# Performance work log

Measured on AMD Instinct MI355X. Metric: run time of the kernel, lower is better.

The kernel has to match this reference:

```python
import math
import jax, jax.numpy as jnp
import numpy as np

WS = 4            # window size
LS = 2 * WS       # local context size
NH = 8            # num heads
DIM = 128
EPS = 1e-5


def setup_inputs() -> dict:
    key = jax.random.key(0)
    ks = jax.random.split(key, 8)
    B, C, H, W = 4, DIM, 48, 48
    features = jax.random.normal(ks[0], (B, C, H, W), dtype=jnp.float32)
    s = 0.02
    return {
        'features': features,
        'ln_w': jnp.ones((C,), jnp.float32),
        'ln_b': jnp.zeros((C,), jnp.float32),
        'q_w': jax.random.normal(ks[1], (C, C), jnp.float32) * s,
        'q_b': jnp.zeros((C,), jnp.float32),
        'kv_w': jax.random.normal(ks[2], (2 * C, C), jnp.float32) * s,
        'kv_b': jnp.zeros((2 * C,), jnp.float32),
        'out_w': jax.random.normal(ks[3], (C, C), jnp.float32) * s,
        'out_b': jnp.zeros((C,), jnp.float32),
    }


def _avgpool_tokens(x, k):
    # x: [B,C,H,W] -> [B, (H//k)*(W//k), C]
    B, C, H, W = x.shape
    t = x.reshape(B, C, H // k, k, W // k, k).mean(axis=(3, 5))
    return t.reshape(B, C, -1).transpose(0, 2, 1)


def reference(features, ln_w, ln_b, q_w, q_b, kv_w, kv_b, out_w, out_b):
    B, C, H, W = features.shape
    Hw, Ww = H // WS, W // WS
    nw = Hw * Ww
    hd = C // NH

    # ---- window partition: [B,C,H,W] -> [B*nw, WS*WS, C]
    qt = features.reshape(B, C, Hw, WS, Ww, WS).transpose(0, 2, 4, 3, 5, 1)
    qt = qt.reshape(B * nw, WS * WS, C)

    # ---- LayerNorm(dim)
    mu = qt.mean(-1, keepdims=True)
    var = qt.var(-1, keepdims=True)
    qt = (qt - mu) / jnp.sqrt(var + EPS) * ln_w + ln_b

    # ---- local context: pad to target, unfold kernel=LS stride=WS
    target = (int(math.sqrt(nw)) - 1) * WS + LS
    ph, pw = max(0, target - H), max(0, target - W)
    pad = ((0, 0), (0, 0), (ph // 2, ph - ph // 2), (pw // 2, pw - pw // 2))
    padded = jnp.pad(features, pad)
    # channel order of patches is (C, kh, kw), same as torch unfold
    patches = jax.lax.conv_general_dilated_patches(
        padded, filter_shape=(LS, LS), window_strides=(WS, WS), padding='VALID')
    local = patches.reshape(B, C, LS * LS, nw).transpose(0, 3, 2, 1)
    local = local.reshape(B * nw, LS * LS, C)

    # ---- multi-scale pooled tokens, broadcast to each window
    mid = _avgpool_tokens(features, 2)      # [B, M, C]
    glo = _avgpool_tokens(features, 4)      # [B, G, C]
    mid = jnp.broadcast_to(mid[:, None], (B, nw) + mid.shape[1:]).reshape(B * nw, -1, C)
    glo = jnp.broadcast_to(glo[:, None], (B, nw) + glo.shape[1:]).reshape(B * nw, -1, C)

    kv_tokens = jnp.concatenate([local, mid, glo], axis=1)  # [B*nw, Nkv, C]

    # ---- projections (torch Linear: x @ W.T + b)
    queries = qt @ q_w.T + q_b
    kv = kv_tokens @ kv_w.T + kv_b
    keys, values = kv[..., :C], kv[..., C:]

    # ---- multi-head attention
    Nq, Nkv = queries.shape[1], keys.shape[1]
    q = queries.reshape(-1, Nq, NH, hd)
    k = keys.reshape(-1, Nkv, NH, hd)
    v = values.reshape(-1, Nkv, NH, hd)
    scores = jnp.einsum('bqhd,bkhd->bhqk', q, k) / math.sqrt(hd)
    weights = jax.nn.softmax(scores, axis=-1)
    attended = jnp.einsum('bhqk,bkhd->bqhd', weights, v).reshape(-1, Nq, C)

    out = attended @ out_w.T + out_b

    # ---- window reconstruction -> [B,C,H,W]
    out = out.reshape(B, Hw, Ww, WS, WS, C).transpose(0, 5, 1, 3, 2, 4)
    out = out.reshape(B, C, H, W)
    return out + features
```

## Files before the change

kernel.cpp:

```cpp
#include <hip/hip_runtime.h>


typedef unsigned short u16;
typedef short v8s __attribute__((ext_vector_type(8)));
typedef v8s __attribute__((may_alias)) v8s_am;
typedef short v4s __attribute__((ext_vector_type(4)));
typedef v4s __attribute__((may_alias)) v4s_am;
typedef float v4f __attribute__((ext_vector_type(4)));

#define MFMA_BF16(a, b, c) __builtin_amdgcn_mfma_f32_16x16x32_bf16(a, b, c, 0, 0, 0)

#if __has_builtin(__builtin_amdgcn_mfma_f32_16x16x16bf16_1k)
#define MFMA16(a, b, c) __builtin_amdgcn_mfma_f32_16x16x16bf16_1k(a, b, c, 0, 0, 0)
#else
static __device__ __forceinline__ v4f mfma16_fb(v4s a, v4s b, v4f c) {
    v8s a8 = {a[0], a[1], a[2], a[3], 0, 0, 0, 0};
    v8s b8 = {b[0], b[1], b[2], b[3], 0, 0, 0, 0};
    return MFMA_BF16(a8, b8, c);
}
#define MFMA16(a, b, c) mfma16_fb(a, b, c)
#endif

#if __has_builtin(__builtin_amdgcn_exp2f)
#define EXP2(x) __builtin_amdgcn_exp2f(x)
#else
#define EXP2(x) exp2f(x)
#endif

__device__ __forceinline__ float b2f(u16 u) {
    union { unsigned int i; float f; } x;
    x.i = ((unsigned int)u) << 16;
    return x.f;
}
__device__ __forceinline__ u16 f2b(float f) {
    union { float f; unsigned int i; } x;
    x.f = f;
    unsigned int u = x.i;
    return (u16)((u + 0x7fffu + ((u >> 16) & 1u)) >> 16);
}

__global__ __launch_bounds__(256) void k_prep(
    const float* __restrict__ F,
    const float* __restrict__ qw, const float* __restrict__ kvw,
    const float* __restrict__ ow,
    const float* __restrict__ lnw, const float* __restrict__ lnb,
    u16* __restrict__ Xt, u16* __restrict__ Wb, float* __restrict__ MuRs,
    u16* __restrict__ Pml)
{
    int blk = blockIdx.x;
    int t = threadIdx.x;
    if (blk >= 304) {
        int gid = (blk - 304) * 256 + t;
        int row = gid >> 4;
        int seg = gid & 15;
        v8s outv;
        if (row < 2304) {
            int b = row / 576, r = row % 576;
            int i = r / 24, j = r % 24;
#pragma unroll
            for (int jc = 0; jc < 8; ++jc) {
                int c = seg * 8 + jc;
                const float* src = F + ((size_t)(b * 128 + c)) * 2304 + (2 * i) * 48 + 2 * j;
                float2 a = *(const float2*)src;
                float2 d = *(const float2*)(src + 48);
                outv[jc] = (short)f2b((a.x + a.y + d.x + d.y) * 0.25f);
            }
        } else {
            int r2 = row - 2304;
            int b = r2 / 144, r = r2 % 144;
            int i = r / 12, j = r % 12;
#pragma unroll
            for (int jc = 0; jc < 8; ++jc) {
                int c = seg * 8 + jc;
                const float* src = F + ((size_t)(b * 128 + c)) * 2304 + (4 * i) * 48 + 4 * j;
                float s = 0.f;
#pragma unroll
                for (int di = 0; di < 4; ++di) {
                    float4 v = *(const float4*)(src + di * 48);
                    s += (v.x + v.y) + (v.z + v.w);
                }
                outv[jc] = (short)f2b(s * 0.0625f);
            }
        }
        *(v8s_am*)&Pml[((size_t)row) * 128 + seg * 8] = outv;
        return;
    }
    if (blk >= 288) {
        int base = (blk - 288) * 4096 + t * 16;
#pragma unroll
        for (int i = 0; i < 4; ++i) {
            int idx = base + i * 4;
            const float* src; int off;
            if (idx < 16384)      { src = qw;  off = idx; }
            else if (idx < 49152) { src = kvw; off = idx - 16384; }
            else                  { src = ow;  off = idx - 49152; }
            float4 v = *(const float4*)(src + off);
            unsigned long long packed =
                (unsigned long long)f2b(v.x) |
                ((unsigned long long)f2b(v.y) << 16) |
                ((unsigned long long)f2b(v.z) << 32) |
                ((unsigned long long)f2b(v.w) << 48);
            *(unsigned long long*)(Wb + idx) = packed;
        }
        if (blk == 288) {
            Wb[65536 + t] = f2b(t < 128 ? lnw[t] : lnb[t - 128]);
        }
        return;
    }
    __shared__ u16 X[128][34];
    int b = blk / 72;
    int p0 = (blk % 72) * 32;
#pragma unroll 4
    for (int i = 0; i < 16; ++i) {
        int c = i * 8 + (t >> 5);
        int pix = t & 31;
        X[c][pix] = f2b(F[((size_t)(b * 128 + c)) * 2304 + p0 + pix]);
    }
    __syncthreads();
    int pix = t >> 3;
    int c0 = (t & 7) * 16;
    size_t row = (size_t)(b * 2304 + p0 + pix) * 128;
    float s = 0.f, s2 = 0.f;
#pragma unroll
    for (int sg = 0; sg < 2; ++sg) {
        v8s raw;
#pragma unroll
        for (int j = 0; j < 8; ++j) {
            u16 u = X[c0 + sg * 8 + j][pix];
            raw[j] = (short)u;
            float v = b2f(u);
            s += v; s2 += v * v;
        }
        *(v8s_am*)&Xt[row + c0 + sg * 8] = raw;
    }
    s += __shfl_xor(s, 1);  s2 += __shfl_xor(s2, 1);
    s += __shfl_xor(s, 2);  s2 += __shfl_xor(s2, 2);
    s += __shfl_xor(s, 4);  s2 += __shfl_xor(s2, 4);
    if ((t & 7) == 0) {
        float mean = s * (1.f / 128.f);
        float var = s2 * (1.f / 128.f) - mean * mean;
        float rstd = rsqrtf(var + 1e-5f);
        MuRs[(b * 2304 + p0 + pix) * 2]     = mean;
        MuRs[(b * 2304 + p0 + pix) * 2 + 1] = rstd;
    }
}

__global__ __launch_bounds__(256) void k_gemm_kv(
    const u16* __restrict__ Pml,
    const u16* __restrict__ W,
    const float* __restrict__ bias,
    u16* __restrict__ KVh,
    u16* __restrict__ VTg)
{
    __shared__ u16 Al[64][136];
    __shared__ u16 Wl[64][136];
    int tm = blockIdx.x * 64, tn = blockIdx.y * 64;
    int t = threadIdx.x;
    {
        int seg = t & 15, r0 = t >> 4;
#pragma unroll
        for (int i = 0; i < 4; ++i) {
            int r = r0 + 16 * i;
            *(v8s_am*)&Al[r][seg * 8] = *(const v8s_am*)&Pml[((size_t)(tm + r)) * 128 + seg * 8];
            *(v8s_am*)&Wl[r][seg * 8] = *(const v8s_am*)&W[((size_t)(tn + r)) * 128 + seg * 8];
        }
    }
    __syncthreads();
    int lane = t & 63, wave = t >> 6;
    int n15 = lane & 15, quad = lane >> 4;
    int wm = (wave & 1) * 32, wn = (wave >> 1) * 32;
    v4f acc[2][2] = {};
#pragma unroll
    for (int kc = 0; kc < 4; ++kc) {
        v8s a[2], bb[2];
#pragma unroll
        for (int im = 0; im < 2; ++im)
            a[im] = *(const v8s_am*)&Al[wm + im * 16 + n15][kc * 32 + quad * 8];
#pragma unroll
        for (int in = 0; in < 2; ++in)
            bb[in] = *(const v8s_am*)&Wl[wn + in * 16 + n15][kc * 32 + quad * 8];
#pragma unroll
        for (int im = 0; im < 2; ++im)
#pragma unroll
            for (int in = 0; in < 2; ++in)
                acc[im][in] = MFMA_BF16(a[im], bb[in], acc[im][in]);
    }
#pragma unroll
    for (int in = 0; in < 2; ++in) {
        int n = tn + wn + in * 16 + n15;
        float bv = bias[n];
#pragma unroll
        for (int im = 0; im < 2; ++im) {
            int mbase = tm + wm + im * 16 + quad * 4;
#pragma unroll
            for (int r = 0; r < 4; ++r) {
                int m = mbase + r;
                u16 h = f2b(acc[im][in][r] + bv);
                if (n < 128) {
                    KVh[((size_t)(n >> 4) * 2880 + m) * 16 + (n & 15)] = h;
                } else {
                    int ch = n - 128, bb2, tok;
                    if (m < 2304) { bb2 = m / 576; tok = m % 576; }
                    else { int r2 = m - 2304; bb2 = r2 / 144; tok = 576 + r2 % 144; }
                    VTg[((size_t)(bb2 * 128 + ch)) * 720 + tok] = h;
                }
            }
        }
    }
}

__global__ __launch_bounds__(512, 2) void k_attn_fused(
    const float* __restrict__ F,
    const u16* __restrict__ Xt,
    const float* __restrict__ MuRs,
    const u16* __restrict__ KVh,
    const u16* __restrict__ VTg,
    const u16* __restrict__ Wb,
    const float* __restrict__ qb,
    const float* __restrict__ kvb,
    const float* __restrict__ ob,
    float* __restrict__ Out)
{
    __shared__ u16 KP[8][64][16];
    __shared__ u16 VtW[8][16][68];

    const u16* qwb  = Wb;
    const u16* kvwb = Wb + 16384;
    const u16* owb  = Wb + 49152;
    const u16* lnwb = Wb + 65536;
    const u16* lnbb = Wb + 65664;
    u16* Atp = &VtW[0][0][0];

    int blk = blockIdx.x;
    int xcd = blk & 7, jj = blk >> 3;
    int b = xcd >> 1;
    int wr = (xcd & 1) * 6 + jj / 12;
    int wc = jj % 12;

    int t = threadIdx.x;
    int lane = t & 63, wave = t >> 6, n15 = lane & 15, quad = lane >> 4;
    v8s zf8 = {};
    v4f zz4 = {0.f, 0.f, 0.f, 0.f};
    const float QSCALE = 0.25f * 1.44269504f;

    u16* KPw = &KP[wave][0][0];
    const u16* kwave = KVh + (size_t)wave * 46080;
    const u16* vrow0 = VTg + (size_t)b * 92160
                     + (size_t)(wave * 16 + n15) * 720 + quad * 4;

    v8s kN0, kN1;
    {
        const u16* s = kwave + (size_t)(b * 576 + lane) * 16;
        kN0 = *(const v8s_am*)s; kN1 = *(const v8s_am*)(s + 8);
    }

    int qh = wr * 4 + (n15 >> 2), qw_ = wc * 4 + (n15 & 3);
    int qpix = b * 2304 + qh * 48 + qw_;
    float mu = MuRs[qpix * 2], rstd = MuRs[qpix * 2 + 1];
    v8s xln[4];
#pragma unroll
    for (int kc = 0; kc < 4; ++kc) {
        v8s x  = *(const v8s_am*)&Xt[(size_t)qpix * 128 + kc * 32 + quad * 8];
        v8s lw = *(const v8s_am*)&lnwb[kc * 32 + quad * 8];
        v8s lb = *(const v8s_am*)&lnbb[kc * 32 + quad * 8];
        v8s y;
#pragma unroll
        for (int j = 0; j < 8; ++j)
            y[j] = (short)f2b((b2f((u16)x[j]) - mu) * rstd * b2f((u16)lw[j]) + b2f((u16)lb[j]));
        xln[kc] = y;
    }

    v4s qf;
    {
        int n0 = wave * 16;
        v4f qacc = zz4;
#pragma unroll
        for (int kc = 0; kc < 4; ++kc) {
            v8s aw = *(const v8s_am*)&qwb[((size_t)(n0 + n15)) * 128 + kc * 32 + quad * 8];
            qacc = MFMA_BF16(aw, xln[kc], qacc);
        }
#pragma unroll
        for (int r = 0; r < 4; ++r)
            qf[r] = (short)f2b((qacc[r] + qb[n0 + quad * 4 + r]) * QSCALE);
    }

    v4s kfloc[4];
#pragma unroll
    for (int g = 0; g < 4; ++g) {
        int tl = g * 16 + n15;
        int fh = tl >> 3, fw = tl & 7;
        int hh = wr * 4 - 2 + fh, ww = wc * 4 - 2 + fw;
        bool valid = (hh >= 0 && hh < 48 && ww >= 0 && ww < 48);
        size_t arow = (size_t)(b * 2304 + hh * 48 + ww) * 128;
        v8s xb[4];
#pragma unroll
        for (int kc = 0; kc < 4; ++kc) {
            v8s v = zf8;
            if (valid) v = *(const v8s_am*)&Xt[arow + kc * 32 + quad * 8];
            xb[kc] = v;
        }
#pragma unroll
        for (int s = 0; s < 2; ++s) {
            int sbase = s * 128 + wave * 16;
            v4f acc = zz4;
#pragma unroll
            for (int kc = 0; kc < 4; ++kc) {
                v8s aw = *(const v8s_am*)&kvwb[((size_t)(sbase + n15)) * 128 + kc * 32 + quad * 8];
                acc = MFMA_BF16(aw, xb[kc], acc);
            }
            if (s == 0) {
                v4s k4;
#pragma unroll
                for (int r = 0; r < 4; ++r)
                    k4[r] = (short)f2b(acc[r] + kvb[sbase + quad * 4 + r]);
                kfloc[g] = k4;
            } else {
#pragma unroll
                for (int r = 0; r < 4; ++r)
                    VtW[wave][quad * 4 + r][g * 16 + n15] =
                        f2b(acc[r] + kvb[sbase + quad * 4 + r]);
            }
        }
    }

    v4f oacc = zz4;
    float ls = 0.f;

    asm volatile("s_waitcnt lgkmcnt(0)" ::: "memory");
#pragma unroll
    for (int g = 0; g < 4; ++g) {
        v4f St = MFMA16(kfloc[g], qf, zz4);
        float p0 = EXP2(St[0]), p1 = EXP2(St[1]);
        float p2 = EXP2(St[2]), p3 = EXP2(St[3]);
        ls += (p0 + p1) + (p2 + p3);
        v4s pk = {(short)f2b(p0), (short)f2b(p1), (short)f2b(p2), (short)f2b(p3)};
        v4s vf = *(const v4s_am*)&VtW[wave][n15][g * 16 + quad * 4];
        oacc = MFMA16(vf, pk, oacc);
    }
    __syncthreads();

    *(v8s_am*)&KPw[lane * 16]     = kN0;
    *(v8s_am*)&KPw[lane * 16 + 8] = kN1;
    {
        const u16* s = kwave + (size_t)(b * 576 + 64 + lane) * 16;
        kN0 = *(const v8s_am*)s; kN1 = *(const v8s_am*)(s + 8);
    }

    for (int tb = 0; tb <= 10; ++tb) {
        v4s kf[4];
#pragma unroll
        for (int g = 0; g < 4; ++g)
            kf[g] = *(const v4s_am*)&KPw[(g * 16 + n15) * 16 + quad * 4];
        *(v8s_am*)&KPw[lane * 16]     = kN0;
        *(v8s_am*)&KPw[lane * 16 + 8] = kN1;
        if (tb < 10) {
            int t2 = tb + 2;
            int row = (t2 < 9) ? (b * 576 + t2 * 64 + lane)
                               : (2304 + b * 144 + (t2 - 9) * 64 + lane);
            if (t2 == 11) row = 2304 + b * 144 + 128 + n15;
            const u16* s = kwave + (size_t)row * 16;
            kN0 = *(const v8s_am*)s; kN1 = *(const v8s_am*)(s + 8);
        }
        v4s vp[4];
#pragma unroll
        for (int g = 0; g < 4; ++g)
            vp[g] = *(const v4s_am*)(vrow0 + tb * 64 + g * 16);
#pragma unroll
        for (int g = 0; g < 4; ++g) {
            v4f St = MFMA16(kf[g], qf, zz4);
            float p0 = EXP2(St[0]), p1 = EXP2(St[1]);
            float p2 = EXP2(St[2]), p3 = EXP2(St[3]);
            ls += (p0 + p1) + (p2 + p3);
            v4s pk = {(short)f2b(p0), (short)f2b(p1), (short)f2b(p2), (short)f2b(p3)};
            oacc = MFMA16(vp[g], pk, oacc);
        }
    }
    {
        v4s kf = *(const v4s_am*)&KPw[n15 * 16 + quad * 4];
        v4s vf = *(const v4s_am*)(vrow0 + 704);
        v4f St = MFMA16(kf, qf, zz4);
        float p0 = EXP2(St[0]), p1 = EXP2(St[1]);
        float p2 = EXP2(St[2]), p3 = EXP2(St[3]);
        ls += (p0 + p1) + (p2 + p3);
        v4s pk = {(short)f2b(p0), (short)f2b(p1), (short)f2b(p2), (short)f2b(p3)};
        oacc = MFMA16(vf, pk, oacc);
    }

    ls += __shfl_xor(ls, 16);
    ls += __shfl_xor(ls, 32);
    {
        float inv = 1.f / ls;
        v4s a4 = {(short)f2b(oacc[0] * inv), (short)f2b(oacc[1] * inv),
                  (short)f2b(oacc[2] * inv), (short)f2b(oacc[3] * inv)};
        *(v4s_am*)&Atp[n15 * 136 + wave * 16 + quad * 4] = a4;
    }
    __syncthreads();

    {
        int n0 = wave * 16;
        v4f oa = zz4;
#pragma unroll
        for (int kc = 0; kc < 4; ++kc) {
            v8s af = *(const v8s_am*)&Atp[n15 * 136 + kc * 32 + quad * 8];
            v8s bf = *(const v8s_am*)&owb[((size_t)(n0 + n15)) * 128 + kc * 32 + quad * 8];
            oa = MFMA_BF16(af, bf, oa);
        }
        int c = n0 + n15;
        float bv = ob[c];
#pragma unroll
        for (int r = 0; r < 4; ++r) {
            int pix = quad * 4 + r;
            int hh = wr * 4 + (pix >> 2), ww_ = wc * 4 + (pix & 3);
            size_t idx = ((size_t)(b * 128 + c)) * 2304 + hh * 48 + ww_;
            Out[idx] = oa[r] + bv + F[idx];
        }
    }
}

extern "C" void kernel_launch(void* const* d_in, const int* in_sizes, int n_in,
                              void* d_out, int out_size, void* d_ws, size_t ws_size,
                              hipStream_t stream)
{
    const float* F   = (const float*)d_in[0];
    const float* lnw = (const float*)d_in[1];
    const float* lnb = (const float*)d_in[2];
    const float* qw  = (const float*)d_in[3];
    const float* qb  = (const float*)d_in[4];
    const float* kvw = (const float*)d_in[5];
    const float* kvb = (const float*)d_in[6];
    const float* ow  = (const float*)d_in[7];
    const float* ob  = (const float*)d_in[8];
    float* Out = (float*)d_out;

    u16* ws    = (u16*)d_ws;
    u16* Xt    = ws;
    u16* Pml   = Xt + 9216 * 128;
    u16* KVh   = Pml + 2880 * 128;
    u16* VTg   = KVh + 8 * 2880 * 16;
    u16* Wb    = VTg + 4 * 128 * 720;
    float* MuRs = (float*)(Wb + 65792);
    u16* kvwb = Wb + 16384;

    k_prep<<<484, 256, 0, stream>>>(F, qw, kvw, ow, lnw, lnb, Xt, Wb, MuRs, Pml);
    k_gemm_kv<<<dim3(45, 4), 256, 0, stream>>>(Pml, kvwb, kvb, KVh, VTg);
    k_attn_fused<<<576, 512, 0, stream>>>(F, Xt, MuRs, KVh, VTg, Wb,
                                          qb, kvb, ob, Out);
}
```

Baseline: 129.1 us.

## Swizzle K LDS staging, prefetch V one tile ahead, raise occupancy bound

After: 131.7 us. 2.0% more time.

```diff
diff --git a/kernel.cpp b/kernel.cpp
--- a/kernel.cpp
+++ b/kernel.cpp
@@ -209,7 +209,7 @@
     }
 }
 
-__global__ __launch_bounds__(512, 2) void k_attn_fused(
+__global__ __launch_bounds__(512, 3) void k_attn_fused(
     const float* __restrict__ F,
     const u16* __restrict__ Xt,
     const float* __restrict__ MuRs,
@@ -243,7 +243,12 @@
     v4f zz4 = {0.f, 0.f, 0.f, 0.f};
     const float QSCALE = 0.25f * 1.44269504f;
 
-    u16* KPw = &KP[wave][0][0];
+    char* KPb = (char*)&KP[wave][0][0];
+    int swW = (lane & 7) << 4;
+    int wb0 = (lane * 32) ^ swW;
+    int wb1 = (lane * 32 + 16) ^ swW;
+    int rdb = (n15 * 32 + quad * 8) ^ ((n15 & 7) << 4);
+
     const u16* kwave = KVh + (size_t)wave * 46080;
     const u16* vrow0 = VTg + (size_t)b * 92160
                      + (size_t)(wave * 16 + n15) * 720 + quad * 4;
@@ -339,20 +344,23 @@
     }
     __syncthreads();
 
-    *(v8s_am*)&KPw[lane * 16]     = kN0;
-    *(v8s_am*)&KPw[lane * 16 + 8] = kN1;
+    *(v8s_am*)(KPb + wb0) = kN0;
+    *(v8s_am*)(KPb + wb1) = kN1;
     {
         const u16* s = kwave + (size_t)(b * 576 + 64 + lane) * 16;
         kN0 = *(const v8s_am*)s; kN1 = *(const v8s_am*)(s + 8);
     }
+    v4s vpC[4], vpN[4];
+#pragma unroll
+    for (int g = 0; g < 4; ++g) vpC[g] = *(const v4s_am*)(vrow0 + g * 16);
 
     for (int tb = 0; tb <= 10; ++tb) {
         v4s kf[4];
 #pragma unroll
         for (int g = 0; g < 4; ++g)
-            kf[g] = *(const v4s_am*)&KPw[(g * 16 + n15) * 16 + quad * 4];
-        *(v8s_am*)&KPw[lane * 16]     = kN0;
-        *(v8s_am*)&KPw[lane * 16 + 8] = kN1;
+            kf[g] = *(const v4s_am*)(KPb + rdb + g * 512);
+        *(v8s_am*)(KPb + wb0) = kN0;
+        *(v8s_am*)(KPb + wb1) = kN1;
         if (tb < 10) {
             int t2 = tb + 2;
             int row = (t2 < 9) ? (b * 576 + t2 * 64 + lane)
@@ -361,10 +369,14 @@
             const u16* s = kwave + (size_t)row * 16;
             kN0 = *(const v8s_am*)s; kN1 = *(const v8s_am*)(s + 8);
         }
-        v4s vp[4];
-#pragma unroll
-        for (int g = 0; g < 4; ++g)
-            vp[g] = *(const v4s_am*)(vrow0 + tb * 64 + g * 16);
+        {
+            int o1 = (tb == 10) ? 704 : (tb + 1) * 64;
+#pragma unroll
+            for (int g = 0; g < 4; ++g) {
+                int off = (tb == 10) ? 704 : (o1 + g * 16);
+                vpN[g] = *(const v4s_am*)(vrow0 + off);
+            }
+        }
 #pragma unroll
         for (int g = 0; g < 4; ++g) {
             v4f St = MFMA16(kf[g], qf, zz4);
@@ -372,18 +384,19 @@
             float p2 = EXP2(St[2]), p3 = EXP2(St[3]);
             ls += (p0 + p1) + (p2 + p3);
             v4s pk = {(short)f2b(p0), (short)f2b(p1), (short)f2b(p2), (short)f2b(p3)};
-            oacc = MFMA16(vp[g], pk, oacc);
-        }
-    }
-    {
-        v4s kf = *(const v4s_am*)&KPw[n15 * 16 + quad * 4];
-        v4s vf = *(const v4s_am*)(vrow0 + 704);
+            oacc = MFMA16(vpC[g], pk, oacc);
+        }
+#pragma unroll
+        for (int g = 0; g < 4; ++g) vpC[g] = vpN[g];
+    }
+    {
+        v4s kf = *(const v4s_am*)(KPb + rdb);
         v4f St = MFMA16(kf, qf, zz4);
         float p0 = EXP2(St[0]), p1 = EXP2(St[1]);
         float p2 = EXP2(St[2]), p3 = EXP2(St[3]);
         ls += (p0 + p1) + (p2 + p3);
         v4s pk = {(short)f2b(p0), (short)f2b(p1), (short)f2b(p2), (short)f2b(p3)};
-        oacc = MFMA16(vf, pk, oacc);
+        oacc = MFMA16(vpC[0], pk, oacc);
     }
 
     ls += __shfl_xor(ls, 16);
```

## Precompute local K/V projection per pixel once instead of per window

Applied to the files above, without the earlier changes.

New measurement: 121.6 us. 5.8% less time.

```diff
diff --git a/kernel.cpp b/kernel.cpp
--- a/kernel.cpp
+++ b/kernel.cpp
@@ -44,11 +44,25 @@
     const float* __restrict__ qw, const float* __restrict__ kvw,
     const float* __restrict__ ow,
     const float* __restrict__ lnw, const float* __restrict__ lnb,
+    const float* __restrict__ kvb,
     u16* __restrict__ Xt, u16* __restrict__ Wb, float* __restrict__ MuRs,
-    u16* __restrict__ Pml)
+    u16* __restrict__ Pml, u16* __restrict__ Vlh)
 {
     int blk = blockIdx.x;
     int t = threadIdx.x;
+    if (blk >= 484) {
+        int base = (blk - 484) * 8192 + t * 32;
+#pragma unroll
+        for (int k = 0; k < 4; ++k) {
+            int off = base + k * 8;
+            int ch = off / 10816;
+            u16 bv = f2b(kvb[128 + ch]);
+            v8s o = {(short)bv, (short)bv, (short)bv, (short)bv,
+                     (short)bv, (short)bv, (short)bv, (short)bv};
+            *(v8s_am*)&Vlh[off] = o;
+        }
+        return;
+    }
     if (blk >= 304) {
         int gid = (blk - 304) * 256 + t;
         int row = gid >> 4;
@@ -104,6 +118,7 @@
         }
         if (blk == 288) {
             Wb[65536 + t] = f2b(t < 128 ? lnw[t] : lnb[t - 128]);
+            Wb[65792 + t] = f2b(kvb[t]);
         }
         return;
     }
@@ -146,22 +161,29 @@
 }
 
 __global__ __launch_bounds__(256) void k_gemm_kv(
+    const u16* __restrict__ Xt,
     const u16* __restrict__ Pml,
     const u16* __restrict__ W,
     const float* __restrict__ bias,
     u16* __restrict__ KVh,
-    u16* __restrict__ VTg)
+    u16* __restrict__ VTg,
+    u16* __restrict__ Klh,
+    u16* __restrict__ Vlh)
 {
     __shared__ u16 Al[64][136];
     __shared__ u16 Wl[64][136];
-    int tm = blockIdx.x * 64, tn = blockIdx.y * 64;
+    int gb = blockIdx.x;
+    bool loc = (gb < 144);
+    int tm = loc ? gb * 64 : (gb - 144) * 64;
+    int tn = blockIdx.y * 64;
     int t = threadIdx.x;
     {
         int seg = t & 15, r0 = t >> 4;
+        const u16* A = loc ? Xt : Pml;
 #pragma unroll
         for (int i = 0; i < 4; ++i) {
             int r = r0 + 16 * i;
-            *(v8s_am*)&Al[r][seg * 8] = *(const v8s_am*)&Pml[((size_t)(tm + r)) * 128 + seg * 8];
+            *(v8s_am*)&Al[r][seg * 8] = *(const v8s_am*)&A[((size_t)(tm + r)) * 128 + seg * 8];
             *(v8s_am*)&Wl[r][seg * 8] = *(const v8s_am*)&W[((size_t)(tn + r)) * 128 + seg * 8];
         }
     }
@@ -196,40 +218,51 @@
             for (int r = 0; r < 4; ++r) {
                 int m = mbase + r;
                 u16 h = f2b(acc[im][in][r] + bv);
-                if (n < 128) {
-                    KVh[((size_t)(n >> 4) * 2880 + m) * 16 + (n & 15)] = h;
+                if (loc) {
+                    int b = m / 2304, px = m % 2304;
+                    if (n < 128) {
+                        Klh[(((size_t)(n >> 4) * 4 + b) * 2304 + px) * 16 + (n & 15)] = h;
+                    } else {
+                        int ch = n - 128;
+                        int hh = px / 48, ww = px % 48;
+                        Vlh[((size_t)(ch * 4 + b)) * 2704 + (hh + 2) * 52 + ww + 2] = h;
+                    }
                 } else {
-                    int ch = n - 128, bb2, tok;
-                    if (m < 2304) { bb2 = m / 576; tok = m % 576; }
-                    else { int r2 = m - 2304; bb2 = r2 / 144; tok = 576 + r2 % 144; }
-                    VTg[((size_t)(bb2 * 128 + ch)) * 720 + tok] = h;
+                    if (n < 128) {
+                        KVh[((size_t)(n >> 4) * 2880 + m) * 16 + (n & 15)] = h;
+                    } else {
+                        int ch = n - 128, bb2, tok;
+                        if (m < 2304) { bb2 = m / 576; tok = m % 576; }
+                        else { int r2 = m - 2304; bb2 = r2 / 144; tok = 576 + r2 % 144; }
+                        VTg[((size_t)(bb2 * 128 + ch)) * 720 + tok] = h;
+                    }
                 }
             }
         }
     }
 }
 
-__global__ __launch_bounds__(512, 2) void k_attn_fused(
+__global__ __launch_bounds__(512, 3) void k_attn_fused(
     const float* __restrict__ F,
     const u16* __restrict__ Xt,
     const float* __restrict__ MuRs,
     const u16* __restrict__ KVh,
     const u16* __restrict__ VTg,
+    const u16* __restrict__ Klh,
+    const u16* __restrict__ Vlh,
     const u16* __restrict__ Wb,
     const float* __restrict__ qb,
-    const float* __restrict__ kvb,
     const float* __restrict__ ob,
     float* __restrict__ Out)
 {
     __shared__ u16 KP[8][64][16];
-    __shared__ u16 VtW[8][16][68];
+    __shared__ u16 At[16][136];
 
     const u16* qwb  = Wb;
-    const u16* kvwb = Wb + 16384;
     const u16* owb  = Wb + 49152;
     const u16* lnwb = Wb + 65536;
     const u16* lnbb = Wb + 65664;
-    u16* Atp = &VtW[0][0][0];
+    const u16* kvbb = Wb + 65792;
 
     int blk = blockIdx.x;
     int xcd = blk & 7, jj = blk >> 3;
@@ -239,7 +272,6 @@
 
     int t = threadIdx.x;
     int lane = t & 63, wave = t >> 6, n15 = lane & 15, quad = lane >> 4;
-    v8s zf8 = {};
     v4f zz4 = {0.f, 0.f, 0.f, 0.f};
     const float QSCALE = 0.25f * 1.44269504f;
 
@@ -248,9 +280,13 @@
     const u16* vrow0 = VTg + (size_t)b * 92160
                      + (size_t)(wave * 16 + n15) * 720 + quad * 4;
 
+    int fh = lane >> 3, fw = lane & 7;
+    int hh = wr * 4 - 2 + fh, ww = wc * 4 - 2 + fw;
+    bool kvalid = (hh >= 0 && hh < 48 && ww >= 0 && ww < 48);
+    int hc = min(max(hh, 0), 47), wcc = min(max(ww, 0), 47);
     v8s kN0, kN1;
     {
-        const u16* s = kwave + (size_t)(b * 576 + lane) * 16;
+        const u16* s = Klh + ((size_t)((wave * 4 + b) * 2304 + hc * 48 + wcc)) * 16;
         kN0 = *(const v8s_am*)s; kN1 = *(const v8s_am*)(s + 8);
     }
 
@@ -284,60 +320,37 @@
             qf[r] = (short)f2b((qacc[r] + qb[n0 + quad * 4 + r]) * QSCALE);
     }
 
-    v4s kfloc[4];
-#pragma unroll
-    for (int g = 0; g < 4; ++g) {
-        int tl = g * 16 + n15;
-        int fh = tl >> 3, fw = tl & 7;
-        int hh = wr * 4 - 2 + fh, ww = wc * 4 - 2 + fw;
-        bool valid = (hh >= 0 && hh < 48 && ww >= 0 && ww < 48);
-        size_t arow = (size_t)(b * 2304 + hh * 48 + ww) * 128;
-        v8s xb[4];
-#pragma unroll
-        for (int kc = 0; kc < 4; ++kc) {
-            v8s v = zf8;
-            if (valid) v = *(const v8s_am*)&Xt[arow + kc * 32 + quad * 8];
-            xb[kc] = v;
-        }
-#pragma unroll
-        for (int s = 0; s < 2; ++s) {
-            int sbase = s * 128 + wave * 16;
-            v4f acc = zz4;
-#pragma unroll
-            for (int kc = 0; kc < 4; ++kc) {
-                v8s aw = *(const v8s_am*)&kvwb[((size_t)(sbase + n15)) * 128 + kc * 32 + quad * 8];
-                acc = MFMA_BF16(aw, xb[kc], acc);
-            }
-            if (s == 0) {
-                v4s k4;
-#pragma unroll
-                for (int r = 0; r < 4; ++r)
-                    k4[r] = (short)f2b(acc[r] + kvb[sbase + quad * 4 + r]);
-                kfloc[g] = k4;
-            } else {
-#pragma unroll
-                for (int r = 0; r < 4; ++r)
-                    VtW[wave][quad * 4 + r][g * 16 + n15] =
-                        f2b(acc[r] + kvb[sbase + quad * 4 + r]);
-            }
-        }
+    {
+        v8s kb0 = *(const v8s_am*)&kvbb[wave * 16];
+        v8s kb1 = *(const v8s_am*)&kvbb[wave * 16 + 8];
+        if (!kvalid) { kN0 = kb0; kN1 = kb1; }
     }
 
     v4f oacc = zz4;
     float ls = 0.f;
 
-    asm volatile("s_waitcnt lgkmcnt(0)" ::: "memory");
-#pragma unroll
-    for (int g = 0; g < 4; ++g) {
-        v4f St = MFMA16(kfloc[g], qf, zz4);
-        float p0 = EXP2(St[0]), p1 = EXP2(St[1]);
-        float p2 = EXP2(St[2]), p3 = EXP2(St[3]);
-        ls += (p0 + p1) + (p2 + p3);
-        v4s pk = {(short)f2b(p0), (short)f2b(p1), (short)f2b(p2), (short)f2b(p3)};
-        v4s vf = *(const v4s_am*)&VtW[wave][n15][g * 16 + quad * 4];
-        oacc = MFMA16(vf, pk, oacc);
-    }
-    __syncthreads();
+    *(v8s_am*)&KPw[lane * 16]     = kN0;
+    *(v8s_am*)&KPw[lane * 16 + 8] = kN1;
+    {
+        const u16* s = kwave + (size_t)(b * 576 + lane) * 16;
+        kN0 = *(const v8s_am*)s; kN1 = *(const v8s_am*)(s + 8);
+    }
+
+    {
+        const u16* vbaseL = Vlh + ((size_t)((wave * 16 + n15) * 4 + b)) * 2704
+                          + (wr * 4 + (quad >> 1)) * 52 + wc * 4 + (quad & 1) * 4;
+#pragma unroll
+        for (int g = 0; g < 4; ++g) {
+            v4s kf = *(const v4s_am*)&KPw[(g * 16 + n15) * 16 + quad * 4];
+            v4s vf = *(const v4s_am*)(vbaseL + g * 104);
+            v4f St = MFMA16(kf, qf, zz4);
+            float p0 = EXP2(St[0]), p1 = EXP2(St[1]);
+            float p2 = EXP2(St[2]), p3 = EXP2(St[3]);
+            ls += (p0 + p1) + (p2 + p3);
+            v4s pk = {(short)f2b(p0), (short)f2b(p1), (short)f2b(p2), (short)f2b(p3)};
+            oacc = MFMA16(vf, pk, oacc);
+        }
+    }
 
     *(v8s_am*)&KPw[lane * 16]     = kN0;
     *(v8s_am*)&KPw[lane * 16 + 8] = kN1;
@@ -392,7 +405,7 @@
         float inv = 1.f / ls;
         v4s a4 = {(short)f2b(oacc[0] * inv), (short)f2b(oacc[1] * inv),
                   (short)f2b(oacc[2] * inv), (short)f2b(oacc[3] * inv)};
-        *(v4s_am*)&Atp[n15 * 136 + wave * 16 + quad * 4] = a4;
+        *(v4s_am*)&At[n15][wave * 16 + quad * 4] = a4;
     }
     __syncthreads();
 
@@ -401,7 +414,7 @@
         v4f oa = zz4;
 #pragma unroll
         for (int kc = 0; kc < 4; ++kc) {
-            v8s af = *(const v8s_am*)&Atp[n15 * 136 + kc * 32 + quad * 8];
+            v8s af = *(const v8s_am*)&At[n15][kc * 32 + quad * 8];
             v8s bf = *(const v8s_am*)&owb[((size_t)(n0 + n15)) * 128 + kc * 32 + quad * 8];
             oa = MFMA_BF16(af, bf, oa);
         }
@@ -410,8 +423,8 @@
 #pragma unroll
         for (int r = 0; r < 4; ++r) {
             int pix = quad * 4 + r;
-            int hh = wr * 4 + (pix >> 2), ww_ = wc * 4 + (pix & 3);
-            size_t idx = ((size_t)(b * 128 + c)) * 2304 + hh * 48 + ww_;
+            int hh2 = wr * 4 + (pix >> 2), ww2 = wc * 4 + (pix & 3);
+            size_t idx = ((size_t)(b * 128 + c)) * 2304 + hh2 * 48 + ww2;
             Out[idx] = oa[r] + bv + F[idx];
         }
     }
@@ -437,12 +450,16 @@
     u16* Pml   = Xt + 9216 * 128;
     u16* KVh   = Pml + 2880 * 128;
     u16* VTg   = KVh + 8 * 2880 * 16;
-    u16* Wb    = VTg + 4 * 128 * 720;
-    float* MuRs = (float*)(Wb + 65792);
+    u16* Klh   = VTg + 4 * 128 * 720;
+    u16* Vlh   = Klh + 8 * 4 * 2304 * 16;
+    u16* Wb    = Vlh + 128 * 4 * 2704;
+    float* MuRs = (float*)(Wb + 66048);
     u16* kvwb = Wb + 16384;
 
-    k_prep<<<484, 256, 0, stream>>>(F, qw, kvw, ow, lnw, lnb, Xt, Wb, MuRs, Pml);
-    k_gemm_kv<<<dim3(45, 4), 256, 0, stream>>>(Pml, kvwb, kvb, KVh, VTg);
-    k_attn_fused<<<576, 512, 0, stream>>>(F, Xt, MuRs, KVh, VTg, Wb,
-                                          qb, kvb, ob, Out);
-}
+    k_prep<<<653, 256, 0, stream>>>(F, qw, kvw, ow, lnw, lnb, kvb,
+                                    Xt, Wb, MuRs, Pml, Vlh);
+    k_gemm_kv<<<dim3(189, 4), 256, 0, stream>>>(Xt, Pml, kvwb, kvb,
+                                                KVh, VTg, Klh, Vlh);
+    k_attn_fused<<<576, 512, 0, stream>>>(F, Xt, MuRs, KVh, VTg, Klh, Vlh,
+                                          Wb, qb, ob, Out);
+}
```
